# Kernel optimization log

Hardware: AMD Instinct MI355X
Metric: run time of the kernel (lower is better)

## Reference

```python
import jax, jax.numpy as jnp
import numpy as np

IM_SIZE = (32, 32)
SIGMA = 5.0


def gaussian_2d_kernel(size, sigma):
    # Faithful port of the torch helper (meshgrid indexing='ij' over (W,H); square grid here).
    x_coords = jnp.arange(size[1], dtype=jnp.float32)
    y_coords = jnp.arange(size[0], dtype=jnp.float32)
    grid_x, grid_y = jnp.meshgrid(x_coords, y_coords, indexing='ij')
    center = (np.array(size, dtype=np.float32) - 1.0) / 2.0
    dist_sq = (grid_x - center[1]) ** 2 + (grid_y - center[0]) ** 2
    kernel_2d = jnp.exp(-0.5 * dist_sq / (sigma ** 2))
    return kernel_2d / kernel_2d.sum()


def setup_inputs() -> dict:
    rng = jax.random.key(0)
    k1, k2, k3 = jax.random.split(rng, 3)
    B, nH, T, H, W, C = 4, 4, 64, IM_SIZE[0], IM_SIZE[1], 8
    shape = (B, nH, T, H, W, C)
    return {
        'query': jax.random.normal(k1, shape, dtype=jnp.float32),
        'key': jax.random.normal(k2, shape, dtype=jnp.float32),
        'value': jax.random.normal(k3, shape, dtype=jnp.float32),
    }


def reference(query, key, value):
    B, nH, T, H, W, C = query.shape
    scale = jnp.float32(H * W)  # sqrt((H*W)^2)
    gauss_2d = gaussian_2d_kernel(IM_SIZE, SIGMA)  # [H, W] (square)
    # k_x: linear dot over flattened (H,W,C)
    q = query.reshape(B, nH, T, -1)
    k = key.reshape(B, nH, T, -1)
    dot_2d = jnp.einsum('bnpf,bnqf->bnpq', q, k) / scale  # [B,nH,T,T]
    # Original builds operator_val[b,n,p,q,h,w] = dot_2d[b,n,p,q]*gauss[h,w] then
    # contracts over q; the rank-1 Gaussian factors out of the q-contraction exactly:
    # out[b,n,p,m,d] = gauss_flat[m] * sum_q dot_2d[b,n,p,q] * val[b,n,q,m,d].
    val_2d = value.reshape(B, nH, T, H * W, -1)  # [B,nH,T,HW,d]
    out_2d = jnp.einsum('bnpq,bnqmd->bnpmd', dot_2d, val_2d)
    out_2d = out_2d * gauss_2d.reshape(1, 1, 1, H * W, 1)
    return out_2d.reshape(B, nH, T, H, W, -1)
```

## Files before the change

### kernel.cpp

```cpp
#include <hip/hip_runtime.h>
#include <cmath>

typedef __bf16 bf16x8 __attribute__((ext_vector_type(8)));
typedef float f32x4 __attribute__((ext_vector_type(4)));
typedef float f32x2 __attribute__((ext_vector_type(2)));

#define HEADS 16
#define TT 64
#define FDIM 8192
#define NCHUNK 32
#define CHUNKF 256

__global__ __launch_bounds__(256) void qk_partial(const float* __restrict__ Q,
                                                  const float* __restrict__ Km,
                                                  float* __restrict__ part) {
    const int chunk = blockIdx.x;
    const int h     = blockIdx.y;
    const int lane  = threadIdx.x & 63;
    const int w     = threadIdx.x >> 6;
    const int pr    = (w & 1) << 5;
    const int qr    = (w >> 1) << 5;
    const int r16   = lane & 15;
    const int g     = lane >> 4;
    const int kb    = (chunk << 8) + (g << 3);

    const float4* qp = (const float4*)(Q  + ((size_t)h * TT + pr + r16) * FDIM + kb);
    const float4* kp = (const float4*)(Km + ((size_t)h * TT + qr + r16) * FDIM + kb);

    f32x4 acc[2][2] = {{{0.f,0.f,0.f,0.f},{0.f,0.f,0.f,0.f}},
                       {{0.f,0.f,0.f,0.f},{0.f,0.f,0.f,0.f}}};

    #pragma unroll
    for (int ks = 0; ks < 8; ++ks) {
        bf16x8 a[2], b[2];
        #pragma unroll
        for (int t = 0; t < 2; ++t) {
            const float4 x0 = qp[(size_t)t * 32768 + ks * 8];
            const float4 x1 = qp[(size_t)t * 32768 + ks * 8 + 1];
            a[t][0]=(__bf16)x0.x; a[t][1]=(__bf16)x0.y; a[t][2]=(__bf16)x0.z; a[t][3]=(__bf16)x0.w;
            a[t][4]=(__bf16)x1.x; a[t][5]=(__bf16)x1.y; a[t][6]=(__bf16)x1.z; a[t][7]=(__bf16)x1.w;
            const float4 y0 = kp[(size_t)t * 32768 + ks * 8];
            const float4 y1 = kp[(size_t)t * 32768 + ks * 8 + 1];
            b[t][0]=(__bf16)y0.x; b[t][1]=(__bf16)y0.y; b[t][2]=(__bf16)y0.z; b[t][3]=(__bf16)y0.w;
            b[t][4]=(__bf16)y1.x; b[t][5]=(__bf16)y1.y; b[t][6]=(__bf16)y1.z; b[t][7]=(__bf16)y1.w;
        }
        #pragma unroll
        for (int i = 0; i < 2; ++i)
            #pragma unroll
            for (int j = 0; j < 2; ++j)
                acc[i][j] = __builtin_amdgcn_mfma_f32_16x16x32_bf16(a[i], b[j], acc[i][j], 0, 0, 0);
    }

    float* pp = part + ((size_t)chunk * HEADS + h) * (TT * TT);
    #pragma unroll
    for (int i = 0; i < 2; ++i)
        #pragma unroll
        for (int j = 0; j < 2; ++j)
            #pragma unroll
            for (int r = 0; r < 4; ++r)
                pp[(pr + (i << 4) + (g << 2) + r) * TT + (qr + (j << 4) + r16)] = acc[i][j][r];
}

__global__ __launch_bounds__(256) void reduce_s(const float* __restrict__ part,
                                                float* __restrict__ St) {
    const int e = blockIdx.x * 256 + threadIdx.x;
    const int h = e >> 12;
    const int r = e & 4095;
    float s = 0.f;
    #pragma unroll
    for (int c = 0; c < NCHUNK; ++c)
        s += part[((size_t)c * HEADS + h) * (TT * TT) + r];
    const int p = r >> 6, q = r & 63;
    St[h * (TT * TT) + q * TT + p] = s * (1.0f / 1024.0f);
}

__global__ __launch_bounds__(256) void sv_out(const float* __restrict__ V,
                                              const float* __restrict__ St,
                                              float* __restrict__ out,
                                              const float g_norm) {
    const int h    = blockIdx.y;
    const int tid  = threadIdx.x;
    const int lane = tid & 63;
    const int w    = tid >> 6;
    const int col  = blockIdx.x * 128 + ((w >> 1) << 6) + lane;
    const int pbase = (w & 1) << 5;
    const int sbase = __builtin_amdgcn_readfirstlane(h * (TT * TT) + pbase);

    const float* Vh = V + (size_t)h * TT * FDIM + col;

    f32x2 acc[16];
    #pragma unroll
    for (int p2 = 0; p2 < 16; ++p2) acc[p2] = (f32x2){0.f, 0.f};

    for (int q0 = 0; q0 < TT; q0 += 8) {
        float v[8];
        #pragma unroll
        for (int i = 0; i < 8; ++i) v[i] = Vh[(size_t)(q0 + i) * FDIM];
        #pragma unroll
        for (int i = 0; i < 8; ++i) {
            const f32x2* S2 = (const f32x2*)(St + sbase + (q0 + i) * TT);
            const f32x2 vv = {v[i], v[i]};
            #pragma unroll
            for (int p2 = 0; p2 < 16; ++p2)
                acc[p2] += S2[p2] * vv;
        }
    }

    const int m   = col >> 3;
    const float dx = (float)(m >> 5) - 15.5f;
    const float dy = (float)(m & 31) - 15.5f;
    const float gg = expf(-(dx * dx + dy * dy) * 0.02f) * g_norm;

    float* O = out + (size_t)h * TT * FDIM + col;
    #pragma unroll
    for (int p2 = 0; p2 < 16; ++p2) {
        O[(size_t)(pbase + 2 * p2)     * FDIM] = acc[p2].x * gg;
        O[(size_t)(pbase + 2 * p2 + 1) * FDIM] = acc[p2].y * gg;
    }
}

extern "C" void kernel_launch(void* const* d_in, const int* in_sizes, int n_in,
                              void* d_out, int out_size, void* d_ws, size_t ws_size,
                              hipStream_t stream) {
    const float* Q  = (const float*)d_in[0];
    const float* Km = (const float*)d_in[1];
    const float* V  = (const float*)d_in[2];
    float* out  = (float*)d_out;
    float* part = (float*)d_out;
    float* St   = (float*)d_ws;

    double sx = 0.0;
    for (int x = 0; x < 32; ++x) { const double d = (double)x - 15.5; sx += exp(-d * d / 50.0); }
    const float g_norm = (float)(1.0 / (sx * sx));

    qk_partial<<<dim3(NCHUNK, HEADS), 256, 0, stream>>>(Q, Km, part);
    reduce_s<<<dim3((HEADS * TT * TT) / 256), 256, 0, stream>>>(part, St);
    sv_out<<<dim3(FDIM / 128, HEADS), 256, 0, stream>>>(V, St, out, g_norm);
}
```

Before: 45.45 us.

## Use bf16 MFMA for S·V and double the QK split-K chunk count

The S·V stage now runs on bf16 MFMA instructions. The reduction kernel stores S in bf16, untransposed, and each wave loads its A fragments straight from it. The QK split-K goes from 32 to 64 chunks of half the width, raising block count and parallelism for the first kernel. In exchange, V and S are rounded to bf16, which adds precision error, and the reduction now sums twice as many partials.

Result: slower. 53.28 us (+17.2%).

```diff
diff --git a/kernel.cpp b/kernel.cpp
--- a/kernel.cpp
+++ b/kernel.cpp
@@ -3,13 +3,12 @@
 
 typedef __bf16 bf16x8 __attribute__((ext_vector_type(8)));
 typedef float f32x4 __attribute__((ext_vector_type(4)));
-typedef float f32x2 __attribute__((ext_vector_type(2)));
 
 #define HEADS 16
 #define TT 64
 #define FDIM 8192
-#define NCHUNK 32
-#define CHUNKF 256
+#define NCHUNK 64
+#define CHUNKF 128
 
 __global__ __launch_bounds__(256) void qk_partial(const float* __restrict__ Q,
                                                   const float* __restrict__ Km,
@@ -22,7 +21,7 @@
     const int qr    = (w >> 1) << 5;
     const int r16   = lane & 15;
     const int g     = lane >> 4;
-    const int kb    = (chunk << 8) + (g << 3);
+    const int kb    = chunk * CHUNKF + (g << 3);
 
     const float4* qp = (const float4*)(Q  + ((size_t)h * TT + pr + r16) * FDIM + kb);
     const float4* kp = (const float4*)(Km + ((size_t)h * TT + qr + r16) * FDIM + kb);
@@ -31,7 +30,7 @@
                        {{0.f,0.f,0.f,0.f},{0.f,0.f,0.f,0.f}}};
 
     #pragma unroll
-    for (int ks = 0; ks < 8; ++ks) {
+    for (int ks = 0; ks < 4; ++ks) {
         bf16x8 a[2], b[2];
         #pragma unroll
         for (int t = 0; t < 2; ++t) {
@@ -61,61 +60,69 @@
                 pp[(pr + (i << 4) + (g << 2) + r) * TT + (qr + (j << 4) + r16)] = acc[i][j][r];
 }
 
-__global__ __launch_bounds__(256) void reduce_s(const float* __restrict__ part,
-                                                float* __restrict__ St) {
+__global__ __launch_bounds__(256) void reduce_sb(const float* __restrict__ part,
+                                                 __bf16* __restrict__ Sbf) {
     const int e = blockIdx.x * 256 + threadIdx.x;
-    const int h = e >> 12;
-    const int r = e & 4095;
     float s = 0.f;
     #pragma unroll
     for (int c = 0; c < NCHUNK; ++c)
-        s += part[((size_t)c * HEADS + h) * (TT * TT) + r];
-    const int p = r >> 6, q = r & 63;
-    St[h * (TT * TT) + q * TT + p] = s * (1.0f / 1024.0f);
+        s += part[(size_t)c * (HEADS * TT * TT) + e];
+    Sbf[e] = (__bf16)(s * (1.0f / 1024.0f));
 }
 
-__global__ __launch_bounds__(256) void sv_out(const float* __restrict__ V,
-                                              const float* __restrict__ St,
-                                              float* __restrict__ out,
-                                              const float g_norm) {
+__global__ __launch_bounds__(256) void sv_mfma(const float* __restrict__ V,
+                                               const __bf16* __restrict__ Sbf,
+                                               float* __restrict__ out,
+                                               const float g_norm) {
     const int h    = blockIdx.y;
-    const int tid  = threadIdx.x;
-    const int lane = tid & 63;
-    const int w    = tid >> 6;
-    const int col  = blockIdx.x * 128 + ((w >> 1) << 6) + lane;
-    const int pbase = (w & 1) << 5;
-    const int sbase = __builtin_amdgcn_readfirstlane(h * (TT * TT) + pbase);
+    const int lane = threadIdx.x & 63;
+    const int w    = threadIdx.x >> 6;
+    const int r16  = lane & 15;
+    const int g    = lane >> 4;
+    const int colbase = blockIdx.x * 128 + w * 32;
 
-    const float* Vh = V + (size_t)h * TT * FDIM + col;
+    const __bf16* Sh = Sbf + h * (TT * TT);
+    bf16x8 a[4][2];
+    #pragma unroll
+    for (int pt = 0; pt < 4; ++pt)
+        #pragma unroll
+        for (int ks = 0; ks < 2; ++ks)
+            a[pt][ks] = *(const bf16x8*)(Sh + (pt * 16 + r16) * TT + ks * 32 + g * 8);
 
-    f32x2 acc[16];
+    const float* Vh = V + (size_t)h * TT * FDIM;
+    f32x4 acc[4][2] = {};
+
     #pragma unroll
-    for (int p2 = 0; p2 < 16; ++p2) acc[p2] = (f32x2){0.f, 0.f};
-
-    for (int q0 = 0; q0 < TT; q0 += 8) {
-        float v[8];
+    for (int jt = 0; jt < 2; ++jt) {
         #pragma unroll
-        for (int i = 0; i < 8; ++i) v[i] = Vh[(size_t)(q0 + i) * FDIM];
-        #pragma unroll
-        for (int i = 0; i < 8; ++i) {
-            const f32x2* S2 = (const f32x2*)(St + sbase + (q0 + i) * TT);
-            const f32x2 vv = {v[i], v[i]};
+        for (int ks = 0; ks < 2; ++ks) {
+            float vf[8];
             #pragma unroll
-            for (int p2 = 0; p2 < 16; ++p2)
-                acc[p2] += S2[p2] * vv;
+            for (int i = 0; i < 8; ++i)
+                vf[i] = Vh[(size_t)(ks * 32 + g * 8 + i) * FDIM + colbase + jt * 16 + r16];
+            bf16x8 b;
+            #pragma unroll
+            for (int i = 0; i < 8; ++i) b[i] = (__bf16)vf[i];
+            #pragma unroll
+            for (int pt = 0; pt < 4; ++pt)
+                acc[pt][jt] = __builtin_amdgcn_mfma_f32_16x16x32_bf16(a[pt][ks], b, acc[pt][jt], 0, 0, 0);
         }
     }
 
-    const int m   = col >> 3;
-    const float dx = (float)(m >> 5) - 15.5f;
-    const float dy = (float)(m & 31) - 15.5f;
-    const float gg = expf(-(dx * dx + dy * dy) * 0.02f) * g_norm;
-
-    float* O = out + (size_t)h * TT * FDIM + col;
     #pragma unroll
-    for (int p2 = 0; p2 < 16; ++p2) {
-        O[(size_t)(pbase + 2 * p2)     * FDIM] = acc[p2].x * gg;
-        O[(size_t)(pbase + 2 * p2 + 1) * FDIM] = acc[p2].y * gg;
+    for (int jt = 0; jt < 2; ++jt) {
+        const int col = colbase + jt * 16 + r16;
+        const int m   = col >> 3;
+        const float dx = (float)(m >> 5) - 15.5f;
+        const float dy = (float)(m & 31) - 15.5f;
+        const float gg = expf(-(dx * dx + dy * dy) * 0.02f) * g_norm;
+        #pragma unroll
+        for (int pt = 0; pt < 4; ++pt)
+            #pragma unroll
+            for (int r = 0; r < 4; ++r) {
+                const int p = pt * 16 + (g << 2) + r;
+                out[(size_t)h * TT * FDIM + (size_t)p * FDIM + col] = acc[pt][jt][r] * gg;
+            }
     }
 }
 
@@ -127,13 +134,13 @@
     const float* V  = (const float*)d_in[2];
     float* out  = (float*)d_out;
     float* part = (float*)d_out;
-    float* St   = (float*)d_ws;
+    __bf16* Sbf = (__bf16*)d_ws;
 
     double sx = 0.0;
     for (int x = 0; x < 32; ++x) { const double d = (double)x - 15.5; sx += exp(-d * d / 50.0); }
     const float g_norm = (float)(1.0 / (sx * sx));
 
     qk_partial<<<dim3(NCHUNK, HEADS), 256, 0, stream>>>(Q, Km, part);
-    reduce_s<<<dim3((HEADS * TT * TT) / 256), 256, 0, stream>>>(part, St);
-    sv_out<<<dim3(FDIM / 128, HEADS), 256, 0, stream>>>(V, St, out, g_norm);
+    reduce_sb<<<dim3((HEADS * TT * TT) / 256), 256, 0, stream>>>(part, Sbf);
+    sv_mfma<<<dim3(FDIM / 128, HEADS), 256, 0, stream>>>(V, Sbf, out, g_norm);
 }
```
